# Kernel optimization log

Measured on AMD Instinct MI355X. Metric: run time of the kernel, lower is better.

The kernel has to match this reference:

```python
import jax, jax.numpy as jnp
import numpy as np

D_MODEL = 1024
NUM_HEADS = 16
HEAD_DIM = D_MODEL // NUM_HEADS


def setup_inputs() -> dict:
    key = jax.random.key(0)
    ks = jax.random.split(key, 11)
    B, S = 2, 2048
    s = 1.0 / np.sqrt(D_MODEL)
    inp = {
        'q': jax.random.normal(ks[0], (B, S, D_MODEL), jnp.float32),
        'k': jax.random.normal(ks[1], (B, S, D_MODEL), jnp.float32),
        'v': jax.random.normal(ks[2], (B, S, D_MODEL), jnp.float32),
        'wq': jax.random.normal(ks[3], (D_MODEL, D_MODEL), jnp.float32) * s,
        'bq': jnp.zeros((D_MODEL,), jnp.float32),
        'wk': jax.random.normal(ks[4], (D_MODEL, D_MODEL), jnp.float32) * s,
        'bk': jnp.zeros((D_MODEL,), jnp.float32),
        'wv': jax.random.normal(ks[5], (D_MODEL, D_MODEL), jnp.float32) * s,
        'bv': jnp.zeros((D_MODEL,), jnp.float32),
        'wo': jax.random.normal(ks[6], (D_MODEL, D_MODEL), jnp.float32) * s,
        'bo': jnp.zeros((D_MODEL,), jnp.float32),
    }
    return inp


def _split_heads(x, B):
    # [B, S, D] -> [B, H, S, Hd]
    return x.reshape(B, -1, NUM_HEADS, HEAD_DIM).transpose(0, 2, 1, 3)


def reference(q, k, v, wq, bq, wk, bk, wv, bv, wo, bo):
    B = q.shape[0]
    qh = _split_heads(q @ wq + bq, B)
    kh = _split_heads(k @ wk + bk, B)
    vh = _split_heads(v @ wv + bv, B)
    scale = 1.0 / np.sqrt(HEAD_DIM).astype(np.float32)
    # [B, H, Sq, Sk]
    scores = jnp.einsum('bhqd,bhkd->bhqk', qh, kh) * scale
    probs = jax.nn.softmax(scores, axis=-1)
    out = jnp.einsum('bhqk,bhkd->bhqd', probs, vh)  # [B, H, Sq, Hd]
    out = out.transpose(0, 2, 1, 3).reshape(B, -1, D_MODEL)
    return out @ wo + bo
```

## Files before the change

kernel.cpp:

```cpp
#include <hip/hip_runtime.h>

typedef unsigned short u16;
typedef __bf16 bf16x8 __attribute__((ext_vector_type(8)));
typedef float    f32x4 __attribute__((ext_vector_type(4)));
typedef float   f32x16 __attribute__((ext_vector_type(16)));
typedef u16      u16x8 __attribute__((ext_vector_type(8)));
typedef u16      u16x4 __attribute__((ext_vector_type(4)));
typedef unsigned uint4v __attribute__((ext_vector_type(4)));

#define DM 1024
#define SQ 2048
#define HD 64

__device__ __forceinline__ u16 f2bf(float f) {
    unsigned u = __builtin_bit_cast(unsigned, f);
    u += 0x7FFFu + ((u >> 16) & 1u);
    return (u16)(u >> 16);
}

__device__ __forceinline__ bf16x8 ldsbf(const u16* p) {
    return __builtin_bit_cast(bf16x8, *(const u16x8*)p);
}

__device__ __forceinline__ unsigned cvtpk(float a, float b) {
    unsigned r;
    asm("v_cvt_pk_bf16_f32 %0, %1, %2" : "=v"(r) : "v"(a), "v"(b));
    return r;
}

__device__ __forceinline__ void swap32(unsigned &a, unsigned &b) {
    asm volatile("v_permlane32_swap_b32 %0, %1" : "+v"(a), "+v"(b));
}

__global__ __launch_bounds__(256) void wtrans_kernel(
    const float* __restrict__ w0, const float* __restrict__ w1,
    const float* __restrict__ w2, const float* __restrict__ w3,
    u16* __restrict__ t0, u16* __restrict__ t1,
    u16* __restrict__ t2, u16* __restrict__ t3)
{
    __shared__ float tile[32][33];
    const int z = blockIdx.z;
    const float* W = (z==0) ? w0 : (z==1) ? w1 : (z==2) ? w2 : w3;
    u16* T        = (z==0) ? t0 : (z==1) ? t1 : (z==2) ? t2 : t3;
    const int tx = threadIdx.x & 31, ty = threadIdx.x >> 5;
    const int n0 = blockIdx.x * 32, k0 = blockIdx.y * 32;
#pragma unroll
    for (int i = 0; i < 4; ++i)
        tile[ty + 8*i][tx] = W[(size_t)(k0 + ty + 8*i)*DM + n0 + tx];
    __syncthreads();
#pragma unroll
    for (int i = 0; i < 4; ++i)
        T[(size_t)(n0 + ty + 8*i)*DM + k0 + tx] = f2bf(tile[tx][ty + 8*i]);
}

template<bool AF32, bool OF32, bool VTLAST>
__global__ __launch_bounds__(256) void gemm_kernel(
    const void* __restrict__ a0, const void* __restrict__ a1, const void* __restrict__ a2,
    const u16* __restrict__ w0, const u16* __restrict__ w1, const u16* __restrict__ w2,
    const float* __restrict__ bi0, const float* __restrict__ bi1, const float* __restrict__ bi2,
    void* __restrict__ o0, void* __restrict__ o1, void* __restrict__ o2)
{
    __shared__ __align__(16) u16 As[128*64];
    __shared__ __align__(16) u16 Bs[128*64];
    const int z = blockIdx.z;
    const void* Ap  = (z==0) ? a0 : (z==1) ? a1 : a2;
    const u16*  Wp  = (z==0) ? w0 : (z==1) ? w1 : w2;
    const float* Bp = (z==0) ? bi0 : (z==1) ? bi1 : bi2;
    void* Op        = (z==0) ? o0 : (z==1) ? o1 : o2;

    const int tid  = threadIdx.x;
    const int lane = tid & 63;
    const int wid  = tid >> 6;
    const int m0 = blockIdx.y * 128;
    const int n0 = blockIdx.x * 128;
    const int wr = (wid >> 1) * 64;
    const int wc = (wid & 1) * 64;
    const int g  = lane >> 4;
    const int mm = lane & 15;
    const int srow = tid >> 3;
    const int c8   = tid & 7;

    const f32x4 zero4 = {0.f, 0.f, 0.f, 0.f};
    f32x4 acc[4][4];
#pragma unroll
    for (int i = 0; i < 4; ++i)
#pragma unroll
        for (int j = 0; j < 4; ++j) acc[i][j] = zero4;

    for (int kt = 0; kt < 16; ++kt) {
        const int k0 = kt * 64;
#pragma unroll
        for (int p = 0; p < 4; ++p) {
            const int row  = p*32 + srow;
            const int didx = row*64 + ((c8 ^ (row & 7)) << 3);
            if (AF32) {
                const float* src = (const float*)Ap + (size_t)(m0+row)*DM + k0 + c8*8;
                f32x4 x0 = *(const f32x4*)src;
                f32x4 x1 = *(const f32x4*)(src + 4);
                u16x8 u;
#pragma unroll
                for (int e = 0; e < 4; ++e) { u[e] = f2bf(x0[e]); u[e+4] = f2bf(x1[e]); }
                *(u16x8*)&As[didx] = u;
            } else {
                const u16* src = (const u16*)Ap + (size_t)(m0+row)*DM + k0 + c8*8;
                *(u16x8*)&As[didx] = *(const u16x8*)src;
            }
            const u16* wsrc = Wp + (size_t)(n0+row)*DM + k0 + c8*8;
            *(u16x8*)&Bs[didx] = *(const u16x8*)wsrc;
        }
        __syncthreads();
#pragma unroll
        for (int ks = 0; ks < 2; ++ks) {
            bf16x8 af[4], bfr[4];
#pragma unroll
            for (int rt = 0; rt < 4; ++rt) {
                const int row = wr + rt*16 + mm;
                const int ch  = ks*4 + g;
                af[rt] = ldsbf(&As[row*64 + ((ch ^ (row & 7)) << 3)]);
            }
#pragma unroll
            for (int ct = 0; ct < 4; ++ct) {
                const int row = wc + ct*16 + mm;
                const int ch  = ks*4 + g;
                bfr[ct] = ldsbf(&Bs[row*64 + ((ch ^ (row & 7)) << 3)]);
            }
#pragma unroll
            for (int rt = 0; rt < 4; ++rt)
#pragma unroll
                for (int ct = 0; ct < 4; ++ct)
                    acc[rt][ct] = __builtin_amdgcn_mfma_f32_16x16x32_bf16(
                        af[rt], bfr[ct], acc[rt][ct], 0, 0, 0);
        }
        __syncthreads();
    }
    if (VTLAST && z == 2) {
#pragma unroll
        for (int ct = 0; ct < 4; ++ct) {
            const int col = n0 + wc + ct*16 + mm;
            const float bv = Bp[col];
#pragma unroll
            for (int rt = 0; rt < 4; ++rt) {
                const int row0 = m0 + wr + rt*16 + g*4;
                const int bb = row0 >> 11, s = row0 & (SQ-1);
                u16x4 pk;
#pragma unroll
                for (int r = 0; r < 4; ++r) pk[r] = f2bf(acc[rt][ct][r] + bv);
                *(u16x4*)&((u16*)Op)[(size_t)(bb*DM + col)*SQ + s] = pk;
            }
        }
    } else {
#pragma unroll
        for (int ct = 0; ct < 4; ++ct) {
            const int col = n0 + wc + ct*16 + mm;
            const float bv = Bp[col];
#pragma unroll
            for (int rt = 0; rt < 4; ++rt) {
#pragma unroll
                for (int r = 0; r < 4; ++r) {
                    const int row = m0 + wr + rt*16 + g*4 + r;
                    const float vv = acc[rt][ct][r] + bv;
                    if (OF32) ((float*)Op)[(size_t)row*DM + col] = vv;
                    else      ((u16*) Op)[(size_t)row*DM + col] = f2bf(vv);
                }
            }
        }
    }
}

__global__ __launch_bounds__(512) void attn_kernel(
    const u16* __restrict__ Q, const u16* __restrict__ K,
    const u16* __restrict__ Vt, u16* __restrict__ Z)
{
    __shared__ __align__(16) u16 Kl[2][64*64];
    __shared__ __align__(16) u16 Vl[2][64*64];

    const int tid  = threadIdx.x;
    const int lane = tid & 63;
    const int wid  = tid >> 6;
    const int c    = lane & 31;
    const int hi   = lane >> 5;
    const int q0   = blockIdx.x * 256;
    const int h    = blockIdx.y;
    const int b    = blockIdx.z;
    const int srow = tid >> 3;
    const int c8   = tid & 7;

    const size_t kbase = (size_t)(b*SQ)*DM + h*HD;
    const size_t vbase = (size_t)((b*16 + h)*HD)*SQ;

    bf16x8 qf[4];
    {
        const size_t qoff = (size_t)(b*SQ + q0 + wid*32 + c)*DM + h*HD + hi*8;
#pragma unroll
        for (int ks = 0; ks < 4; ++ks)
            qf[ks] = ldsbf(&Q[qoff + ks*16]);
    }

    f32x16 oacc[2];
#pragma unroll
    for (int dt = 0; dt < 2; ++dt)
#pragma unroll
        for (int r = 0; r < 16; ++r) oacc[dt][r] = 0.f;
    float lsum = 0.f;

    const int stw = srow*64 + ((c8 ^ (srow & 7)) << 3);
    u16x8 kreg = *(const u16x8*)&K [kbase + (size_t)srow*DM + c8*8];
    u16x8 vreg = *(const u16x8*)&Vt[vbase + (size_t)srow*SQ + c8*8];
    *(u16x8*)&Kl[0][stw] = kreg;
    *(u16x8*)&Vl[0][stw] = vreg;

    const float SC = 0.18033688f;

    for (int t = 0; t < SQ/64; ++t) {
        const int cur = t & 1;
        if (t + 1 < SQ/64) {
            kreg = *(const u16x8*)&K [kbase + (size_t)((t+1)*64 + srow)*DM + c8*8];
            vreg = *(const u16x8*)&Vt[vbase + (size_t)srow*SQ + (t+1)*64 + c8*8];
        }
        __syncthreads();

        f32x16 pacc[2];
#pragma unroll
        for (int kt = 0; kt < 2; ++kt)
#pragma unroll
            for (int r = 0; r < 16; ++r) pacc[kt][r] = 0.f;
#pragma unroll
        for (int ks = 0; ks < 4; ++ks) {
#pragma unroll
            for (int kt = 0; kt < 2; ++kt) {
                const int row = kt*32 + c;
                const int ch  = ks*2 + hi;
                bf16x8 kf = ldsbf(&Kl[cur][row*64 + ((ch ^ (row & 7)) << 3)]);
                pacc[kt] = __builtin_amdgcn_mfma_f32_32x32x16_bf16(kf, qf[ks], pacc[kt], 0, 0, 0);
            }
        }

        float ls = 0.f;
#pragma unroll
        for (int kt = 0; kt < 2; ++kt)
#pragma unroll
            for (int r = 0; r < 16; ++r) {
                const float e = __builtin_amdgcn_exp2f(pacc[kt][r] * SC);
                pacc[kt][r] = e;
                ls += e;
            }
        lsum += ls;

        bf16x8 pa[4];
#pragma unroll
        for (int kt = 0; kt < 2; ++kt)
#pragma unroll
            for (int k2 = 0; k2 < 2; ++k2) {
                const int bs = k2*8;
                unsigned u = cvtpk(pacc[kt][bs+0], pacc[kt][bs+1]);
                unsigned v = cvtpk(pacc[kt][bs+2], pacc[kt][bs+3]);
                unsigned w = cvtpk(pacc[kt][bs+4], pacc[kt][bs+5]);
                unsigned x = cvtpk(pacc[kt][bs+6], pacc[kt][bs+7]);
                swap32(u, w);
                swap32(v, x);
                uint4v fr = {u, v, w, x};
                pa[kt*2 + k2] = __builtin_bit_cast(bf16x8, fr);
            }

#pragma unroll
        for (int kp = 0; kp < 4; ++kp) {
#pragma unroll
            for (int dt = 0; dt < 2; ++dt) {
                const int d  = dt*32 + c;
                const int ch = kp*2 + hi;
                bf16x8 vf = ldsbf(&Vl[cur][d*64 + ((ch ^ (d & 7)) << 3)]);
                oacc[dt] = __builtin_amdgcn_mfma_f32_32x32x16_bf16(pa[kp], vf, oacc[dt], 0, 0, 0);
            }
        }

        if (t + 1 < SQ/64) {
            *(u16x8*)&Kl[cur^1][stw] = kreg;
            *(u16x8*)&Vl[cur^1][stw] = vreg;
        }
    }

    lsum += __shfl_xor(lsum, 32, 64);
    const float linv = 1.f / lsum;
    float linvr[16];
#pragma unroll
    for (int r = 0; r < 16; ++r)
        linvr[r] = __shfl(linv, (r & 3) + 8*(r >> 2) + 4*hi, 64);

#pragma unroll
    for (int dt = 0; dt < 2; ++dt)
#pragma unroll
        for (int r = 0; r < 16; ++r) {
            const int qrl = (r & 3) + 8*(r >> 2) + 4*hi;
            const size_t row = (size_t)(b*SQ + q0 + wid*32 + qrl);
            Z[row*DM + h*HD + dt*32 + c] = f2bf(oacc[dt][r] * linvr[r]);
        }
}

extern "C" void kernel_launch(void* const* d_in, const int* in_sizes, int n_in,
                              void* d_out, int out_size, void* d_ws, size_t ws_size,
                              hipStream_t stream)
{
    const float* q  = (const float*)d_in[0];
    const float* k  = (const float*)d_in[1];
    const float* v  = (const float*)d_in[2];
    const float* wq = (const float*)d_in[3];
    const float* bq = (const float*)d_in[4];
    const float* wk = (const float*)d_in[5];
    const float* bk = (const float*)d_in[6];
    const float* wv = (const float*)d_in[7];
    const float* bv = (const float*)d_in[8];
    const float* wo = (const float*)d_in[9];
    const float* bo = (const float*)d_in[10];
    float* out = (float*)d_out;

    char* ws = (char*)d_ws;
    u16* Qb  = (u16*)(ws);
    u16* Kb  = (u16*)(ws + 8388608);
    u16* VtB = (u16*)(ws + 16777216);
    u16* Zb  = (u16*)(ws + 25165824);
    u16* WtQ = (u16*)(ws + 33554432);
    u16* WtK = (u16*)(ws + 35651584);
    u16* WtV = (u16*)(ws + 37748736);
    u16* WtO = (u16*)(ws + 39845888);

    wtrans_kernel<<<dim3(32, 32, 4), 256, 0, stream>>>(
        wq, wk, wv, wo, WtQ, WtK, WtV, WtO);

    gemm_kernel<true, false, true><<<dim3(8, 32, 3), 256, 0, stream>>>(
        (const void*)q, (const void*)k, (const void*)v,
        WtQ, WtK, WtV, bq, bk, bv,
        (void*)Qb, (void*)Kb, (void*)VtB);

    attn_kernel<<<dim3(SQ/256, 16, 2), 512, 0, stream>>>(Qb, Kb, VtB, Zb);

    gemm_kernel<false, true, false><<<dim3(8, 32, 1), 256, 0, stream>>>(
        (const void*)Zb, (const void*)Zb, (const void*)Zb,
        WtO, WtO, WtO, bo, bo, bo,
        (void*)out, (void*)out, (void*)out);
}
```

Before: 145.4 us.

## Pre-convert inputs to bf16, use direct global-to-LDS loads, XCD remap, setprio

Adds a separate kernel that converts q/k/v from fp32 to bf16 up front, so the projection GEMM no longer converts while staging tiles. The GEMM now stages its tiles with global_load_lds, which writes global memory straight into LDS and skips the register round trip. The swizzle is applied on the global address side instead. Work-group IDs are remapped into a 1D grid so neighbouring tiles land on the same XCD. s_setprio is wrapped around the MFMA blocks in both the GEMM and the attention kernel. The cost is an extra kernel launch and an extra read and write pass over the activations.

```diff
diff --git a/kernel.cpp b/kernel.cpp
--- a/kernel.cpp
+++ b/kernel.cpp
@@ -32,6 +32,29 @@
     asm volatile("v_permlane32_swap_b32 %0, %1" : "+v"(a), "+v"(b));
 }
 
+typedef __attribute__((address_space(3))) unsigned lds_u32_t;
+typedef __attribute__((address_space(1))) const unsigned glob_u32_t;
+__device__ __forceinline__ void gl_lds16(const u16* g, u16* l) {
+    __builtin_amdgcn_global_load_lds((glob_u32_t*)g, (lds_u32_t*)l, 16, 0, 0);
+}
+
+__global__ __launch_bounds__(256) void convert_kernel(
+    const float* __restrict__ q, const float* __restrict__ k,
+    const float* __restrict__ v,
+    u16* __restrict__ Qc, u16* __restrict__ Kc, u16* __restrict__ Vc)
+{
+    const int which = blockIdx.x >> 11;
+    const float* src = (which==0) ? q : (which==1) ? k : v;
+    u16* dst         = (which==0) ? Qc : (which==1) ? Kc : Vc;
+    const int off = ((blockIdx.x & 2047) << 11) + threadIdx.x * 8;
+    f32x4 x0 = *(const f32x4*)&src[off];
+    f32x4 x1 = *(const f32x4*)&src[off + 4];
+    u16x8 u;
+#pragma unroll
+    for (int e = 0; e < 4; ++e) { u[e] = f2bf(x0[e]); u[e+4] = f2bf(x1[e]); }
+    *(u16x8*)&dst[off] = u;
+}
+
 __global__ __launch_bounds__(256) void wtrans_kernel(
     const float* __restrict__ w0, const float* __restrict__ w1,
     const float* __restrict__ w2, const float* __restrict__ w3,
@@ -53,32 +76,40 @@
         T[(size_t)(n0 + ty + 8*i)*DM + k0 + tx] = f2bf(tile[tx][ty + 8*i]);
 }
 
-template<bool AF32, bool OF32, bool VTLAST>
+template<bool OF32, bool VTLAST>
 __global__ __launch_bounds__(256) void gemm_kernel(
-    const void* __restrict__ a0, const void* __restrict__ a1, const void* __restrict__ a2,
+    const u16* __restrict__ a0, const u16* __restrict__ a1, const u16* __restrict__ a2,
     const u16* __restrict__ w0, const u16* __restrict__ w1, const u16* __restrict__ w2,
     const float* __restrict__ bi0, const float* __restrict__ bi1, const float* __restrict__ bi2,
     void* __restrict__ o0, void* __restrict__ o1, void* __restrict__ o2)
 {
     __shared__ __align__(16) u16 As[128*64];
     __shared__ __align__(16) u16 Bs[128*64];
-    const int z = blockIdx.z;
-    const void* Ap  = (z==0) ? a0 : (z==1) ? a1 : a2;
+
+    const int cpx  = gridDim.x >> 3;
+    const int wgid = (blockIdx.x & 7) * cpx + (blockIdx.x >> 3);
+    const int z   = wgid >> 8;
+    const int rem = wgid & 255;
+    const int by  = rem >> 3, bx = rem & 7;
+
+    const u16*  Ap  = (z==0) ? a0 : (z==1) ? a1 : a2;
     const u16*  Wp  = (z==0) ? w0 : (z==1) ? w1 : w2;
     const float* Bp = (z==0) ? bi0 : (z==1) ? bi1 : bi2;
     void* Op        = (z==0) ? o0 : (z==1) ? o1 : o2;
 
     const int tid  = threadIdx.x;
     const int lane = tid & 63;
-    const int wid  = tid >> 6;
-    const int m0 = blockIdx.y * 128;
-    const int n0 = blockIdx.x * 128;
-    const int wr = (wid >> 1) * 64;
-    const int wc = (wid & 1) * 64;
+    const int wv   = tid >> 6;
+    const int m0 = by * 128;
+    const int n0 = bx * 128;
+    const int wr = (wv >> 1) * 64;
+    const int wc = (wv & 1) * 64;
     const int g  = lane >> 4;
     const int mm = lane & 15;
-    const int srow = tid >> 3;
-    const int c8   = tid & 7;
+
+    const int l8  = lane >> 3;
+    const int chs = (lane & 7) ^ l8;
+    const int lrow = wv*8 + l8;
 
     const f32x4 zero4 = {0.f, 0.f, 0.f, 0.f};
     f32x4 acc[4][4];
@@ -90,23 +121,10 @@
     for (int kt = 0; kt < 16; ++kt) {
         const int k0 = kt * 64;
 #pragma unroll
-        for (int p = 0; p < 4; ++p) {
-            const int row  = p*32 + srow;
-            const int didx = row*64 + ((c8 ^ (row & 7)) << 3);
-            if (AF32) {
-                const float* src = (const float*)Ap + (size_t)(m0+row)*DM + k0 + c8*8;
-                f32x4 x0 = *(const f32x4*)src;
-                f32x4 x1 = *(const f32x4*)(src + 4);
-                u16x8 u;
-#pragma unroll
-                for (int e = 0; e < 4; ++e) { u[e] = f2bf(x0[e]); u[e+4] = f2bf(x1[e]); }
-                *(u16x8*)&As[didx] = u;
-            } else {
-                const u16* src = (const u16*)Ap + (size_t)(m0+row)*DM + k0 + c8*8;
-                *(u16x8*)&As[didx] = *(const u16x8*)src;
-            }
-            const u16* wsrc = Wp + (size_t)(n0+row)*DM + k0 + c8*8;
-            *(u16x8*)&Bs[didx] = *(const u16x8*)wsrc;
+        for (int i = 0; i < 4; ++i) {
+            const int row = i*32 + lrow;
+            gl_lds16(&Ap[(size_t)(m0+row)*DM + k0 + chs*8], &As[(i*32 + wv*8)*64]);
+            gl_lds16(&Wp[(size_t)(n0+row)*DM + k0 + chs*8], &Bs[(i*32 + wv*8)*64]);
         }
         __syncthreads();
 #pragma unroll
@@ -124,12 +142,14 @@
                 const int ch  = ks*4 + g;
                 bfr[ct] = ldsbf(&Bs[row*64 + ((ch ^ (row & 7)) << 3)]);
             }
+            __builtin_amdgcn_s_setprio(1);
 #pragma unroll
             for (int rt = 0; rt < 4; ++rt)
 #pragma unroll
                 for (int ct = 0; ct < 4; ++ct)
                     acc[rt][ct] = __builtin_amdgcn_mfma_f32_16x16x32_bf16(
                         af[rt], bfr[ct], acc[rt][ct], 0, 0, 0);
+            __builtin_amdgcn_s_setprio(0);
         }
         __syncthreads();
     }
@@ -224,6 +244,7 @@
         for (int kt = 0; kt < 2; ++kt)
 #pragma unroll
             for (int r = 0; r < 16; ++r) pacc[kt][r] = 0.f;
+        __builtin_amdgcn_s_setprio(1);
 #pragma unroll
         for (int ks = 0; ks < 4; ++ks) {
 #pragma unroll
@@ -234,6 +255,7 @@
                 pacc[kt] = __builtin_amdgcn_mfma_f32_32x32x16_bf16(kf, qf[ks], pacc[kt], 0, 0, 0);
             }
         }
+        __builtin_amdgcn_s_setprio(0);
 
         float ls = 0.f;
 #pragma unroll
@@ -262,6 +284,7 @@
                 pa[kt*2 + k2] = __builtin_bit_cast(bf16x8, fr);
             }
 
+        __builtin_amdgcn_s_setprio(1);
 #pragma unroll
         for (int kp = 0; kp < 4; ++kp) {
 #pragma unroll
@@ -272,6 +295,7 @@
                 oacc[dt] = __builtin_amdgcn_mfma_f32_32x32x16_bf16(pa[kp], vf, oacc[dt], 0, 0, 0);
             }
         }
+        __builtin_amdgcn_s_setprio(0);
 
         if (t + 1 < SQ/64) {
             *(u16x8*)&Kl[cur^1][stw] = kreg;
@@ -314,27 +338,30 @@
     float* out = (float*)d_out;
 
     char* ws = (char*)d_ws;
-    u16* Qb  = (u16*)(ws);
-    u16* Kb  = (u16*)(ws + 8388608);
-    u16* VtB = (u16*)(ws + 16777216);
-    u16* Zb  = (u16*)(ws + 25165824);
-    u16* WtQ = (u16*)(ws + 33554432);
-    u16* WtK = (u16*)(ws + 35651584);
-    u16* WtV = (u16*)(ws + 37748736);
-    u16* WtO = (u16*)(ws + 39845888);
+    u16* Qc  = (u16*)(ws);
+    u16* Kc  = (u16*)(ws + 8388608);
+    u16* Vc  = (u16*)(ws + 16777216);
+    u16* Qb  = (u16*)(ws + 25165824);
+    u16* Kb  = (u16*)(ws + 33554432);
+    u16* VtB = (u16*)(ws + 41943040);
+    u16* WtQ = (u16*)(ws + 50331648);
+    u16* WtK = (u16*)(ws + 52428800);
+    u16* WtV = (u16*)(ws + 54525952);
+    u16* WtO = (u16*)(ws + 56623104);
+    u16* Zb  = Qc;
 
     wtrans_kernel<<<dim3(32, 32, 4), 256, 0, stream>>>(
         wq, wk, wv, wo, WtQ, WtK, WtV, WtO);
 
-    gemm_kernel<true, false, true><<<dim3(8, 32, 3), 256, 0, stream>>>(
-        (const void*)q, (const void*)k, (const void*)v,
-        WtQ, WtK, WtV, bq, bk, bv,
+    convert_kernel<<<dim3(3*2048), 256, 0, stream>>>(q, k, v, Qc, Kc, Vc);
+
+    gemm_kernel<false, true><<<dim3(768), 256, 0, stream>>>(
+        Qc, Kc, Vc, WtQ, WtK, WtV, bq, bk, bv,
         (void*)Qb, (void*)Kb, (void*)VtB);
 
     attn_kernel<<<dim3(SQ/256, 16, 2), 512, 0, stream>>>(Qb, Kb, VtB, Zb);
 
-    gemm_kernel<false, true, false><<<dim3(8, 32, 1), 256, 0, stream>>>(
-        (const void*)Zb, (const void*)Zb, (const void*)Zb,
-        WtO, WtO, WtO, bo, bo, bo,
+    gemm_kernel<true, false><<<dim3(256), 256, 0, stream>>>(
+        Zb, Zb, Zb, WtO, WtO, WtO, bo, bo, bo,
         (void*)out, (void*)out, (void*)out);
 }
```

Result: faster. 128.4 us (-11.7%).
